# Kernel optimization log

Hardware: AMD Instinct MI355X
Metric: run time of the kernel (lower is better)

## Reference

```python
import jax, jax.numpy as jnp
import numpy as np

N_NODES = 100000
N_EDGES = 500000
HIDDEN = 256


def setup_inputs() -> dict:
    key = jax.random.key(0)
    k_x, k_e, k_w1, k_b1, k_w2, k_b2 = jax.random.split(key, 6)
    x = jax.random.normal(k_x, (N_NODES, HIDDEN), dtype=jnp.float32)
    edge_label_index = jax.random.randint(k_e, (2, N_EDGES), 0, N_NODES, dtype=jnp.int64)
    # fc1: Linear(2*hidden -> hidden); fc2: Linear(hidden -> 1). PyTorch stores W as [out, in].
    bound1 = 1.0 / np.sqrt(2 * HIDDEN)
    W1 = jax.random.uniform(k_w1, (HIDDEN, 2 * HIDDEN), dtype=jnp.float32, minval=-bound1, maxval=bound1)
    b1 = jax.random.uniform(k_b1, (HIDDEN,), dtype=jnp.float32, minval=-bound1, maxval=bound1)
    bound2 = 1.0 / np.sqrt(HIDDEN)
    W2 = jax.random.uniform(k_w2, (1, HIDDEN), dtype=jnp.float32, minval=-bound2, maxval=bound2)
    b2 = jax.random.uniform(k_b2, (1,), dtype=jnp.float32, minval=-bound2, maxval=bound2)
    return {"x": x, "edge_label_index": edge_label_index, "W1": W1, "b1": b1, "W2": W2, "b2": b2}


def reference(x, edge_label_index, W1, b1, W2, b2):
    # Gather endpoint features: [E, H] each
    feat_src = x[edge_label_index[0]]
    feat_dst = x[edge_label_index[1]]
    h = jnp.concatenate([feat_src, feat_dst], axis=1)  # [E, 2H]
    h = jax.nn.relu(h @ W1.T + b1)                      # [E, H]
    out = jax.nn.sigmoid(h @ W2.T + b2)                 # [E, 1]
    return out.reshape(-1)
```

## Files before the change

### kernel.cpp

```cpp
#include <hip/hip_runtime.h>
#include <math.h>

#define NNODES 100000
#define MT     64
#define NTILES 1563
#define NODESP (NTILES * MT)
#define NEDGES 500000
#define HID    256
#define K2     512
#define GEMM_GRID 256

typedef _Float16 h8v __attribute__((ext_vector_type(8)));
typedef _Float16 h2v __attribute__((ext_vector_type(2)));
typedef __bf16   bf16x8 __attribute__((ext_vector_type(8)));
typedef float    f32x4  __attribute__((ext_vector_type(4)));

__device__ __forceinline__ unsigned short f2bf(float f) {
    unsigned int u = __float_as_uint(f);
    u += 0x7FFFu + ((u >> 16) & 1u);
    return (unsigned short)(u >> 16);
}

__global__ void cvt_w1h(const float* __restrict__ W1, _Float16* __restrict__ Bsw) {
    int t = blockIdx.x * 256 + threadIdx.x;
    if (t >= 8 * 32 * 64) return;
    int lane = t & 63, nt = (t >> 6) & 31, kt = t >> 11;
    int j = nt * 16 + (lane & 15);
    int k = kt * 32 + ((lane >> 4) << 3);
    const float* src = W1 + (size_t)(j & 255) * K2 + ((j >> 8) << 8) + k;
    union { _Float16 s[8]; uint4 v; } u;
#pragma unroll
    for (int jj = 0; jj < 8; ++jj) u.s[jj] = (_Float16)src[jj];
    ((uint4*)Bsw)[t] = u.v;
}

__global__ void cvt_w2p(const float* __restrict__ W2, float* __restrict__ w2p) {
    int t = threadIdx.x;
    int i = (t >> 2) & 15, nt = t & 3;
    w2p[t] = W2[(t & ~63) | (nt * 16 + i)];
}

__global__ __launch_bounds__(512, 2) void node_gemm4(
    const float* __restrict__ x,
    const _Float16* __restrict__ Bsw,
    const float* __restrict__ b1,
    _Float16* __restrict__ UV)
{
    __shared__ __align__(16) _Float16 Asw[2048 * 8];
    const int tid  = threadIdx.x;
    const int lane = tid & 63;
    const int wave = tid >> 6;

    const h8v* B8 = (const h8v*)Bsw;
    h8v barr[8][4];
#pragma unroll
    for (int ks = 0; ks < 8; ++ks)
#pragma unroll
        for (int nt = 0; nt < 4; ++nt)
            barr[ks][nt] = B8[((size_t)(ks * 32 + wave * 4 + nt)) * 64 + lane];

    float b1v[4];
#pragma unroll
    for (int nt = 0; nt < 4; ++nt) {
        int col = wave * 64 + nt * 16 + (lane & 15);
        b1v[nt] = (col < 256) ? b1[col] : 0.0f;
    }

    uint4* A4 = (uint4*)Asw;
    const h8v* A8 = (const h8v*)Asw;
    const int k8  = tid & 31;
    const int mh  = tid >> 5;
    const int ktl = k8 >> 2, q = k8 & 3;

    auto stage = [&](int tile) {
#pragma unroll
        for (int i = 0; i < 4; ++i) {
            int m   = i * 16 + mh;
            int row = tile * MT + m;
            int rl  = row < NNODES ? row : 0;
            const float4* p = (const float4*)(x + (size_t)rl * 256 + k8 * 8);
            float4 a = p[0], b = p[1];
            union { _Float16 s[8]; uint4 v; } u;
            u.s[0] = (_Float16)a.x; u.s[1] = (_Float16)a.y;
            u.s[2] = (_Float16)a.z; u.s[3] = (_Float16)a.w;
            u.s[4] = (_Float16)b.x; u.s[5] = (_Float16)b.y;
            u.s[6] = (_Float16)b.z; u.s[7] = (_Float16)b.w;
            int logical = (ktl << 8) + ((m >> 4) << 6) + (q << 4) + (m & 15);
            A4[logical ^ ktl] = u.v;
        }
    };

    f32x4 acc[4][4] = {};
    int tile = blockIdx.x;
    if (tile >= NTILES) return;
    stage(tile);
    __syncthreads();

    while (true) {
#pragma unroll
        for (int ks = 0; ks < 8; ++ks) {
            h8v af[4];
#pragma unroll
            for (int mt = 0; mt < 4; ++mt)
                af[mt] = A8[(((ks * 4 + mt) << 6) + lane) ^ ks];
#pragma unroll
            for (int mt = 0; mt < 4; ++mt)
#pragma unroll
                for (int nt = 0; nt < 4; ++nt)
                    acc[mt][nt] = __builtin_amdgcn_mfma_f32_16x16x32_f16(
                        af[mt], barr[ks][nt], acc[mt][nt], 0, 0, 0);
        }
        __syncthreads();

        int next = tile + GEMM_GRID;
        if (next < NTILES) stage(next);

#pragma unroll
        for (int mt = 0; mt < 4; ++mt) {
#pragma unroll
            for (int r = 0; r < 4; ++r) {
                int row = tile * MT + mt * 16 + ((lane >> 4) << 2) + r;
                union { _Float16 h[4]; uint2 v; } pk;
#pragma unroll
                for (int nt = 0; nt < 4; ++nt)
                    pk.h[nt] = (_Float16)(acc[mt][nt][r] + b1v[nt]);
                *(uint2*)(UV + (size_t)row * 512 + wave * 64 + (lane & 15) * 4) = pk.v;
            }
        }
#pragma unroll
        for (int mt = 0; mt < 4; ++mt)
#pragma unroll
            for (int nt = 0; nt < 4; ++nt)
                acc[mt][nt] = f32x4{0.f, 0.f, 0.f, 0.f};

        if (next >= NTILES) break;
        tile = next;
        __syncthreads();
    }
}

__global__ __launch_bounds__(256) void edge_out4(
    const _Float16* __restrict__ UV,
    const int* __restrict__ ei,
    const float* __restrict__ w2p,
    const float* __restrict__ b2,
    float* __restrict__ out)
{
    const int tid = threadIdx.x;
    const int q   = tid & 31;
    const int g   = tid >> 5;
    const long e  = (long)blockIdx.x * 32 + g * 4;

    int4 s4 = *(const int4*)(ei + e);
    int4 d4 = *(const int4*)(ei + NEDGES + e);

    h2v w2h[4];
    {
        const float4* pw = (const float4*)w2p + q * 2;
        float4 c = pw[0], d = pw[1];
        w2h[0] = h2v{(_Float16)c.x, (_Float16)c.y};
        w2h[1] = h2v{(_Float16)c.z, (_Float16)c.w};
        w2h[2] = h2v{(_Float16)d.x, (_Float16)d.y};
        w2h[3] = h2v{(_Float16)d.z, (_Float16)d.w};
    }

    union U8 { uint4 v; h2v h[4]; };
    const _Float16* up = UV + q * 8;

    U8 uu[4], vv[4];
    uu[0].v = *(const uint4*)(up + (size_t)s4.x * 512);
    vv[0].v = *(const uint4*)(up + (size_t)d4.x * 512 + 256);
    uu[1].v = *(const uint4*)(up + (size_t)s4.y * 512);
    vv[1].v = *(const uint4*)(up + (size_t)d4.y * 512 + 256);
    uu[2].v = *(const uint4*)(up + (size_t)s4.z * 512);
    vv[2].v = *(const uint4*)(up + (size_t)d4.z * 512 + 256);
    uu[3].v = *(const uint4*)(up + (size_t)s4.w * 512);
    vv[3].v = *(const uint4*)(up + (size_t)d4.w * 512 + 256);

    const h2v zz = {(_Float16)0.0f, (_Float16)0.0f};
    float z[4] = {0.f, 0.f, 0.f, 0.f};
#pragma unroll
    for (int ed = 0; ed < 4; ++ed) {
#pragma unroll
        for (int p = 0; p < 4; ++p) {
            h2v h = uu[ed].h[p] + vv[ed].h[p];
            h = __builtin_elementwise_max(h, zz);
            z[ed] = __builtin_amdgcn_fdot2(h, w2h[p], z[ed], false);
        }
    }
#pragma unroll
    for (int m = 1; m < 32; m <<= 1) {
        z[0] += __shfl_xor(z[0], m, 32);
        z[1] += __shfl_xor(z[1], m, 32);
        z[2] += __shfl_xor(z[2], m, 32);
        z[3] += __shfl_xor(z[3], m, 32);
    }
    if (q < 4) {
        float zq = (q == 0) ? z[0] : (q == 1) ? z[1] : (q == 2) ? z[2] : z[3];
        out[e + q] = 1.0f / (1.0f + expf(-(zq + b2[0])));
    }
}

__global__ void cvt_w1_r1(const float* __restrict__ W1, unsigned short* __restrict__ Bsw) {
    int t = blockIdx.x * 256 + threadIdx.x;
    if (t >= 16 * 16 * 64) return;
    int lane = t & 63, nt = (t >> 6) & 15, kt = t >> 10;
    int n = nt * 16 + (lane & 15);
    int k = kt * 32 + ((lane >> 4) << 3);
    const float* src = W1 + (size_t)n * K2 + k;
    union { unsigned short s[8]; uint4 v; } u;
#pragma unroll
    for (int j = 0; j < 8; ++j) u.s[j] = f2bf(src[j]);
    ((uint4*)Bsw)[t] = u.v;
}

__global__ __launch_bounds__(256) void edge_mlp_fb(
    const float* __restrict__ xf, const int* __restrict__ ei,
    const unsigned short* __restrict__ Bsw, const float* __restrict__ b1,
    const float* __restrict__ W2, const float* __restrict__ b2,
    float* __restrict__ out)
{
    __shared__ __align__(16) unsigned short Asw[8 * 4 * 64 * 8];
    __shared__ float es[64];
    const int tid = threadIdx.x, lane = tid & 63, wave = tid >> 6;
    const int e0 = blockIdx.x * 64;
    if (tid < 64) es[tid] = 0.0f;
    f32x4 acc[4][4] = {};
    const bf16x8* A8 = (const bf16x8*)Asw;
    const bf16x8* B8 = (const bf16x8*)Bsw;
    for (int h = 0; h < 2; ++h) {
#pragma unroll
        for (int i = 0; i < 8; ++i) {
            int m = i * 8 + wave * 2 + (lane >> 5);
            int e = e0 + m;
            int ee = (e < NEDGES) ? e : 0;
            int node = ei[(size_t)h * NEDGES + ee];
            int chunk = lane & 31;
            const float4* p = (const float4*)(xf + ((size_t)node << 8) + (chunk << 3));
            float4 a = p[0], bq = p[1];
            union { unsigned short s[8]; uint4 v4; } u;
            u.s[0] = f2bf(a.x);  u.s[1] = f2bf(a.y);  u.s[2] = f2bf(a.z);  u.s[3] = f2bf(a.w);
            u.s[4] = f2bf(bq.x); u.s[5] = f2bf(bq.y); u.s[6] = f2bf(bq.z); u.s[7] = f2bf(bq.w);
            int ktl = chunk >> 2, qq = chunk & 3;
            int u16 = ((ktl * 4 + (m >> 4)) << 6) + (qq << 4) + (m & 15);
            u16 ^= (u16 >> 8) & 7;
            ((uint4*)Asw)[u16] = u.v4;
        }
        __syncthreads();
#pragma unroll
        for (int kt = 0; kt < 8; ++kt) {
            bf16x8 af[4], bfr[4];
#pragma unroll
            for (int mt = 0; mt < 4; ++mt) {
                int u16 = ((kt * 4 + mt) << 6) + lane;
                u16 ^= (u16 >> 8) & 7;
                af[mt] = A8[u16];
            }
#pragma unroll
            for (int nt = 0; nt < 4; ++nt)
                bfr[nt] = B8[(((h * 8 + kt) << 4) + (wave << 2) + nt) * 64 + lane];
#pragma unroll
            for (int mt = 0; mt < 4; ++mt)
#pragma unroll
                for (int nt = 0; nt < 4; ++nt)
                    acc[mt][nt] = __builtin_amdgcn_mfma_f32_16x16x32_bf16(
                        af[mt], bfr[nt], acc[mt][nt], 0, 0, 0);
        }
        __syncthreads();
    }
    float w2v[4], b1v[4];
#pragma unroll
    for (int nt = 0; nt < 4; ++nt) {
        int n = (wave << 6) + (nt << 4) + (lane & 15);
        w2v[nt] = W2[n]; b1v[nt] = b1[n];
    }
#pragma unroll
    for (int mt = 0; mt < 4; ++mt) {
#pragma unroll
        for (int r = 0; r < 4; ++r) {
            float p = 0.0f;
#pragma unroll
            for (int nt = 0; nt < 4; ++nt) {
                float hv = acc[mt][nt][r] + b1v[nt];
                p = fmaf(fmaxf(hv, 0.0f), w2v[nt], p);
            }
            p += __shfl_xor(p, 1, 16);
            p += __shfl_xor(p, 2, 16);
            p += __shfl_xor(p, 4, 16);
            p += __shfl_xor(p, 8, 16);
            if ((lane & 15) == 0)
                atomicAdd(&es[(mt << 4) + ((lane >> 4) << 2) + r], p);
        }
    }
    __syncthreads();
    if (tid < 64) {
        int e = e0 + tid;
        if (e < NEDGES) out[e] = 1.0f / (1.0f + expf(-(es[tid] + b2[0])));
    }
}

extern "C" void kernel_launch(void* const* d_in, const int* in_sizes, int n_in,
                              void* d_out, int out_size, void* d_ws, size_t ws_size,
                              hipStream_t stream) {
    const float* x  = (const float*)d_in[0];
    const int*   ei = (const int*)d_in[1];
    const float* W1 = (const float*)d_in[2];
    const float* b1 = (const float*)d_in[3];
    const float* W2 = (const float*)d_in[4];
    const float* b2 = (const float*)d_in[5];
    float* out = (float*)d_out;

    const size_t BSW_BYTES = 1 << 18;
    const size_t W2P_BYTES = 4096;
    const size_t UV_BYTES  = (size_t)NODESP * K2 * 2;
    const size_t NEED_A = BSW_BYTES + W2P_BYTES + UV_BYTES;

    if (ws_size >= NEED_A) {
        _Float16* Bsw = (_Float16*)d_ws;
        float*    w2p = (float*)((char*)d_ws + BSW_BYTES);
        _Float16* UV  = (_Float16*)((char*)d_ws + BSW_BYTES + W2P_BYTES);
        cvt_w1h<<<64, 256, 0, stream>>>(W1, Bsw);
        cvt_w2p<<<1, 256, 0, stream>>>(W2, w2p);
        node_gemm4<<<GEMM_GRID, 512, 0, stream>>>(x, Bsw, b1, UV);
        edge_out4<<<NEDGES / 32, 256, 0, stream>>>(UV, ei, w2p, b2, out);
    } else {
        unsigned short* Bsw = (unsigned short*)d_ws;
        cvt_w1_r1<<<64, 256, 0, stream>>>(W1, Bsw);
        edge_mlp_fb<<<(NEDGES + 63) / 64, 256, 0, stream>>>(x, ei, Bsw, b1, W2, b2, out);
    }
}
```

Before: 253.4 us.

## Double-buffer node GEMM x tiles and gather eight edges per group

The node GEMM now has two LDS buffers. It issues global loads of the next x tile into registers before the MFMA loop and commits them to the alternate buffer afterwards, so the load latency overlaps compute and one barrier per tile is removed. The edge kernel handles eight edges per 32-lane group instead of four, putting more independent gathers in flight and reducing the shuffle reduction per edge. The cost is higher register pressure (prefetch registers alongside 128 B-fragment registers, and 16 uint4 gather buffers), which could cut occupancy or cause spills.

```diff
diff --git a/kernel.cpp b/kernel.cpp
--- a/kernel.cpp
+++ b/kernel.cpp
@@ -40,13 +40,13 @@
     w2p[t] = W2[(t & ~63) | (nt * 16 + i)];
 }
 
-__global__ __launch_bounds__(512, 2) void node_gemm4(
+__global__ __launch_bounds__(512, 2) void node_gemm5(
     const float* __restrict__ x,
     const _Float16* __restrict__ Bsw,
     const float* __restrict__ b1,
     _Float16* __restrict__ UV)
 {
-    __shared__ __align__(16) _Float16 Asw[2048 * 8];
+    __shared__ __align__(16) _Float16 Asw[2][2048 * 8];
     const int tid  = threadIdx.x;
     const int lane = tid & 63;
     const int wave = tid >> 6;
@@ -66,37 +66,50 @@
         b1v[nt] = (col < 256) ? b1[col] : 0.0f;
     }
 
-    uint4* A4 = (uint4*)Asw;
-    const h8v* A8 = (const h8v*)Asw;
     const int k8  = tid & 31;
     const int mh  = tid >> 5;
     const int ktl = k8 >> 2, q = k8 & 3;
 
-    auto stage = [&](int tile) {
+    float4 pa[4], pb[4];
+    auto issue = [&](int tile) {
 #pragma unroll
         for (int i = 0; i < 4; ++i) {
             int m   = i * 16 + mh;
             int row = tile * MT + m;
             int rl  = row < NNODES ? row : 0;
             const float4* p = (const float4*)(x + (size_t)rl * 256 + k8 * 8);
-            float4 a = p[0], b = p[1];
+            pa[i] = p[0];
+            pb[i] = p[1];
+        }
+    };
+    auto commit = [&](int buf) {
+        uint4* A4 = (uint4*)Asw[buf];
+#pragma unroll
+        for (int i = 0; i < 4; ++i) {
+            int m = i * 16 + mh;
             union { _Float16 s[8]; uint4 v; } u;
-            u.s[0] = (_Float16)a.x; u.s[1] = (_Float16)a.y;
-            u.s[2] = (_Float16)a.z; u.s[3] = (_Float16)a.w;
-            u.s[4] = (_Float16)b.x; u.s[5] = (_Float16)b.y;
-            u.s[6] = (_Float16)b.z; u.s[7] = (_Float16)b.w;
+            u.s[0] = (_Float16)pa[i].x; u.s[1] = (_Float16)pa[i].y;
+            u.s[2] = (_Float16)pa[i].z; u.s[3] = (_Float16)pa[i].w;
+            u.s[4] = (_Float16)pb[i].x; u.s[5] = (_Float16)pb[i].y;
+            u.s[6] = (_Float16)pb[i].z; u.s[7] = (_Float16)pb[i].w;
             int logical = (ktl << 8) + ((m >> 4) << 6) + (q << 4) + (m & 15);
             A4[logical ^ ktl] = u.v;
         }
     };
 
-    f32x4 acc[4][4] = {};
     int tile = blockIdx.x;
-    if (tile >= NTILES) return;
-    stage(tile);
+    issue(tile);
+    commit(0);
     __syncthreads();
+    int buf = 0;
 
     while (true) {
+        int next = tile + GEMM_GRID;
+        bool has_next = next < NTILES;
+        if (has_next) issue(next);
+
+        f32x4 acc[4][4] = {};
+        const h8v* A8 = (const h8v*)Asw[buf];
 #pragma unroll
         for (int ks = 0; ks < 8; ++ks) {
             h8v af[4];
@@ -110,10 +123,6 @@
                     acc[mt][nt] = __builtin_amdgcn_mfma_f32_16x16x32_f16(
                         af[mt], barr[ks][nt], acc[mt][nt], 0, 0, 0);
         }
-        __syncthreads();
-
-        int next = tile + GEMM_GRID;
-        if (next < NTILES) stage(next);
 
 #pragma unroll
         for (int mt = 0; mt < 4; ++mt) {
@@ -127,19 +136,16 @@
                 *(uint2*)(UV + (size_t)row * 512 + wave * 64 + (lane & 15) * 4) = pk.v;
             }
         }
-#pragma unroll
-        for (int mt = 0; mt < 4; ++mt)
-#pragma unroll
-            for (int nt = 0; nt < 4; ++nt)
-                acc[mt][nt] = f32x4{0.f, 0.f, 0.f, 0.f};
-
-        if (next >= NTILES) break;
+
+        if (!has_next) break;
+        commit(buf ^ 1);
+        __syncthreads();
+        buf ^= 1;
         tile = next;
-        __syncthreads();
-    }
-}
-
-__global__ __launch_bounds__(256) void edge_out4(
+    }
+}
+
+__global__ __launch_bounds__(256) void edge_out5(
     const _Float16* __restrict__ UV,
     const int* __restrict__ ei,
     const float* __restrict__ w2p,
@@ -149,10 +155,25 @@
     const int tid = threadIdx.x;
     const int q   = tid & 31;
     const int g   = tid >> 5;
-    const long e  = (long)blockIdx.x * 32 + g * 4;
-
-    int4 s4 = *(const int4*)(ei + e);
-    int4 d4 = *(const int4*)(ei + NEDGES + e);
+    const long e  = ((long)blockIdx.x * 8 + g) * 8;
+    if (e >= NEDGES) return;
+
+    int4 s0 = *(const int4*)(ei + e);
+    int4 s1 = *(const int4*)(ei + e + 4);
+    int4 d0 = *(const int4*)(ei + NEDGES + e);
+    int4 d1 = *(const int4*)(ei + NEDGES + e + 4);
+    int is[8] = {s0.x, s0.y, s0.z, s0.w, s1.x, s1.y, s1.z, s1.w};
+    int id[8] = {d0.x, d0.y, d0.z, d0.w, d1.x, d1.y, d1.z, d1.w};
+
+    union U8 { uint4 v; h2v h[4]; };
+    const _Float16* up = UV + q * 8;
+
+    U8 uu[8], vv[8];
+#pragma unroll
+    for (int ed = 0; ed < 8; ++ed) {
+        uu[ed].v = *(const uint4*)(up + (size_t)is[ed] * 512);
+        vv[ed].v = *(const uint4*)(up + (size_t)id[ed] * 512 + 256);
+    }
 
     h2v w2h[4];
     {
@@ -164,39 +185,29 @@
         w2h[3] = h2v{(_Float16)d.z, (_Float16)d.w};
     }
 
-    union U8 { uint4 v; h2v h[4]; };
-    const _Float16* up = UV + q * 8;
-
-    U8 uu[4], vv[4];
-    uu[0].v = *(const uint4*)(up + (size_t)s4.x * 512);
-    vv[0].v = *(const uint4*)(up + (size_t)d4.x * 512 + 256);
-    uu[1].v = *(const uint4*)(up + (size_t)s4.y * 512);
-    vv[1].v = *(const uint4*)(up + (size_t)d4.y * 512 + 256);
-    uu[2].v = *(const uint4*)(up + (size_t)s4.z * 512);
-    vv[2].v = *(const uint4*)(up + (size_t)d4.z * 512 + 256);
-    uu[3].v = *(const uint4*)(up + (size_t)s4.w * 512);
-    vv[3].v = *(const uint4*)(up + (size_t)d4.w * 512 + 256);
-
     const h2v zz = {(_Float16)0.0f, (_Float16)0.0f};
-    float z[4] = {0.f, 0.f, 0.f, 0.f};
-#pragma unroll
-    for (int ed = 0; ed < 4; ++ed) {
+    float z[8];
+#pragma unroll
+    for (int ed = 0; ed < 8; ++ed) {
+        float zt = 0.f;
 #pragma unroll
         for (int p = 0; p < 4; ++p) {
             h2v h = uu[ed].h[p] + vv[ed].h[p];
             h = __builtin_elementwise_max(h, zz);
-            z[ed] = __builtin_amdgcn_fdot2(h, w2h[p], z[ed], false);
-        }
+            zt = __builtin_amdgcn_fdot2(h, w2h[p], zt, false);
+        }
+        z[ed] = zt;
     }
 #pragma unroll
     for (int m = 1; m < 32; m <<= 1) {
-        z[0] += __shfl_xor(z[0], m, 32);
-        z[1] += __shfl_xor(z[1], m, 32);
-        z[2] += __shfl_xor(z[2], m, 32);
-        z[3] += __shfl_xor(z[3], m, 32);
-    }
-    if (q < 4) {
-        float zq = (q == 0) ? z[0] : (q == 1) ? z[1] : (q == 2) ? z[2] : z[3];
+#pragma unroll
+        for (int ed = 0; ed < 8; ++ed)
+            z[ed] += __shfl_xor(z[ed], m, 32);
+    }
+    if (q < 8) {
+        float zq = (q == 0) ? z[0] : (q == 1) ? z[1] : (q == 2) ? z[2] :
+                   (q == 3) ? z[3] : (q == 4) ? z[4] : (q == 5) ? z[5] :
+                   (q == 6) ? z[6] : z[7];
         out[e + q] = 1.0f / (1.0f + expf(-(zq + b2[0])));
     }
 }
@@ -321,8 +332,8 @@
         _Float16* UV  = (_Float16*)((char*)d_ws + BSW_BYTES + W2P_BYTES);
         cvt_w1h<<<64, 256, 0, stream>>>(W1, Bsw);
         cvt_w2p<<<1, 256, 0, stream>>>(W2, w2p);
-        node_gemm4<<<GEMM_GRID, 512, 0, stream>>>(x, Bsw, b1, UV);
-        edge_out4<<<NEDGES / 32, 256, 0, stream>>>(UV, ei, w2p, b2, out);
+        node_gemm5<<<GEMM_GRID, 512, 0, stream>>>(x, Bsw, b1, UV);
+        edge_out5<<<7813, 256, 0, stream>>>(UV, ei, w2p, b2, out);
     } else {
         unsigned short* Bsw = (unsigned short*)d_ws;
         cvt_w1_r1<<<64, 256, 0, stream>>>(W1, Bsw);
```

Measured after the change: 267.3 us. +5.5%, slower.
